# Optimization experiments

Measured on AMD Instinct MI355X. Metric: run time of the kernel, lower is better.

The kernel has to match this reference:

```python
import jax, jax.numpy as jnp
import numpy as np

IN_FEATURES_LS = (32, 64, 128, 256)
OUT_FEATURES = 1024
B, T = 16, 4096


def setup_inputs() -> dict:
    key = jax.random.key(0)
    k_x, k_idx, k_w, k_b = jax.random.split(key, 4)
    n = len(IN_FEATURES_LS)
    x = jax.random.normal(k_x, (B, T, OUT_FEATURES), dtype=jnp.float32)
    # per-row declared feature size, drawn from the configured list
    branch_idx = jax.random.randint(k_idx, (B, T), 0, n)
    in_feat_size = jnp.array(IN_FEATURES_LS, dtype=jnp.int32)[branch_idx]
    # kaiming_uniform_(a=sqrt(5)) on (n, out, out): fan_in = out, bound = 1/sqrt(fan_in)
    bound_w = 1.0 / np.sqrt(OUT_FEATURES)
    weight = jax.random.uniform(k_w, (n, OUT_FEATURES, OUT_FEATURES), dtype=jnp.float32,
                                minval=-bound_w, maxval=bound_w)
    bound_b = 1.0 / np.sqrt(OUT_FEATURES)
    bias = jax.random.uniform(k_b, (n, OUT_FEATURES), dtype=jnp.float32,
                              minval=-bound_b, maxval=bound_b)
    return {"x": x, "in_feat_size": in_feat_size, "weight": weight, "bias": bias}


def reference(x, in_feat_size, weight, bias):
    # Loop over the small fixed set of feature-size branches (matches original).
    out = jnp.zeros(x.shape[:-1] + (OUT_FEATURES,), dtype=x.dtype)
    for idx, feat_size in enumerate(IN_FEATURES_LS):
        mask = (in_feat_size == feat_size)[..., None].astype(x.dtype)  # [B,T,1]
        y = jnp.einsum('oi,bti->bto', weight[idx], x) + bias[idx]
        out = out + mask * y
    return out
```

## Files before the change

kernel.cpp:

```cpp
#include <hip/hip_runtime.h>
#include <hip/hip_bf16.h>

#define OUTF 1024
#define NROWS 65536
#define NBR 4
#define XBROWS 66560
#define NWG 1040

typedef __attribute__((ext_vector_type(8))) short short8;
typedef __attribute__((ext_vector_type(4))) float f32x4;

__device__ inline unsigned short f2bf(float f) {
    return __builtin_bit_cast(unsigned short, (__bf16)f);
}
__device__ inline void gload_lds16(const void* g, void* l) {
    __builtin_amdgcn_global_load_lds(
        (const __attribute__((address_space(1))) void*)g,
        (__attribute__((address_space(3))) void*)l, 16, 0, 0);
}
__device__ inline short8 pack8(float4 a, float4 b) {
    short8 o;
    o[0] = (short)f2bf(a.x); o[1] = (short)f2bf(a.y);
    o[2] = (short)f2bf(a.z); o[3] = (short)f2bf(a.w);
    o[4] = (short)f2bf(b.x); o[5] = (short)f2bf(b.y);
    o[6] = (short)f2bf(b.z); o[7] = (short)f2bf(b.w);
    return o;
}

#define VMCNT(n) asm volatile("s_waitcnt vmcnt(" #n ")" ::: "memory")
#define SBAR() do { __builtin_amdgcn_s_barrier(); __builtin_amdgcn_sched_barrier(0); } while (0)

__global__ void k_count(const int* __restrict__ feat, int* __restrict__ cnt) {
    __shared__ int lc[NBR];
    int tid = threadIdx.x;
    if (tid < NBR) lc[tid] = 0;
    __syncthreads();
    int r = blockIdx.x * 256 + tid;
    int b = 26 - __clz(feat[r]);
    atomicAdd(&lc[b], 1);
    __syncthreads();
    if (tid < NBR && lc[tid]) atomicAdd(&cnt[tid], lc[tid]);
}

__global__ void k_prefix(int* __restrict__ ws) {
    if (threadIdx.x == 0) {
        int s = 0;
        for (int b = 0; b < NBR; b++) {
            ws[4 + b] = s;
            s = (s + ws[b] + 255) & ~255;
            ws[8 + b] = 0;
        }
    }
}

__global__ void k_fill(const int* __restrict__ feat, int* __restrict__ ws,
                       int* __restrict__ rowlist) {
    int tid = threadIdx.x;
    int lane = tid & 63;
    int r = blockIdx.x * 256 + tid;
    int b = 26 - __clz(feat[r]);
    #pragma unroll
    for (int bb = 0; bb < NBR; bb++) {
        unsigned long long mask = __ballot(b == bb);
        int leader = __ffsll((long long)mask) - 1;
        int cntw = __popcll(mask);
        int basepos = 0;
        if (lane == leader) basepos = atomicAdd(&ws[8 + bb], cntw);
        basepos = __shfl(basepos, leader < 0 ? 0 : leader);
        if (b == bb) {
            int prefix = __popcll(mask & ((1ull << lane) - 1ull));
            rowlist[ws[4 + bb] + basepos + prefix] = r;
        }
    }
}

__global__ void k_convw(const float* __restrict__ w, unsigned short* __restrict__ wb) {
    int i = ((int)blockIdx.x * 256 + (int)threadIdx.x) * 8;
    const float4* s = reinterpret_cast<const float4*>(w + i);
    *reinterpret_cast<short8*>(wb + i) = pack8(s[0], s[1]);
}

__global__ void k_convx(const float* __restrict__ x, const int* __restrict__ rowlist,
                        unsigned short* __restrict__ xb) {
    int g = (int)blockIdx.x * 512 + (int)threadIdx.x;
    int orow = g >> 7;
    int cb = (g & 127) << 4;
    int rl = rowlist[orow];
    if ((unsigned)rl >= NROWS) rl = 0;
    const float4* s = reinterpret_cast<const float4*>(x + (size_t)rl * OUTF + (cb >> 1));
    *reinterpret_cast<short8*>(reinterpret_cast<char*>(xb) + (size_t)orow * 2048 + cb) =
        pack8(s[0], s[1]);
}

__global__ __launch_bounds__(512, 2)
void k_gemm6(const unsigned short* __restrict__ xb,
             const unsigned short* __restrict__ wb,
             const float* __restrict__ bias,
             const int* __restrict__ ws_i,
             const int* __restrict__ rowlist,
             float* __restrict__ out) {
    extern __shared__ char lds[];

    const int d = (int)blockIdx.x;
    const int work = (d & 7) * (NWG >> 3) + (d >> 3);
    const int mtile = work >> 2;
    const int ntile = work & 3;

    int branch = -1, lt = 0, cnt = 0, rbase = 0;
    int t_ = mtile;
    #pragma unroll
    for (int b = 0; b < NBR; b++) {
        if (branch < 0) {
            int c = ws_i[b];
            int nt = (c + 255) >> 8;
            if (t_ < nt) { branch = b; lt = t_; cnt = c; rbase = ws_i[4 + b]; }
            else t_ -= nt;
        }
    }
    if (branch < 0) return;

    const int tid = threadIdx.x;
    const int lane = tid & 63;
    const int w8 = tid >> 6;
    const int wm = (w8 >> 2) * 128;
    const int wn = (w8 & 3) * 64;
    const int n0 = ntile * 256;
    const int row0 = rbase + lt * 256;

    const char* aSrc = reinterpret_cast<const char*>(xb)
                       + (size_t)(row0 + (tid >> 2)) * 2048 + ((tid & 3) << 4);
    const char* bSrc = reinterpret_cast<const char*>(wb) + ((size_t)branch << 21)
                       + (size_t)(n0 + (tid >> 2)) * 2048 + ((tid & 3) << 4);
    const int ldst = tid << 4;

    const int aoff = (wm + (lane & 15)) * 64 + ((lane >> 4) << 4);
    const int boff = (wn + (lane & 15)) * 64 + ((lane >> 4) << 4);

    f32x4 acc[8][4];
    #pragma unroll
    for (int i = 0; i < 8; i++)
        #pragma unroll
        for (int j = 0; j < 4; j++) acc[i][j] = (f32x4){0.f, 0.f, 0.f, 0.f};

    #define STAGE(u) do {                                                  \
        const int _sl = (u) % 9;                                           \
        const char* _s = ((u) & 1) ? bSrc : aSrc;                          \
        const int _kb = (((u) >> 2) << 7) + ((((u) >> 1) & 1) << 6);       \
        char* _d = lds + _sl * 16384 + ldst;                               \
        gload_lds16(_s + _kb, _d);                                         \
        gload_lds16(_s + 262144 + _kb, _d + 8192);                         \
    } while (0)

    STAGE(0); STAGE(1); STAGE(2); STAGE(3); STAGE(4); STAGE(5);
    VMCNT(8);
    SBAR();

    short8 af[8], b0, b1;

    for (int t = 0; t < 16; ++t) {
        const int b4 = 4 * t;
        char* A0 = lds + (b4 % 9) * 16384;
        char* B0 = lds + ((b4 + 1) % 9) * 16384;
        char* A1 = lds + ((b4 + 2) % 9) * 16384;
        char* B1 = lds + ((b4 + 3) % 9) * 16384;

        if (t < 15) STAGE(b4 + 6);
        #pragma unroll
        for (int i = 0; i < 8; i++)
            af[i] = *reinterpret_cast<const short8*>(A0 + aoff + i * 1024);
        b0 = *reinterpret_cast<const short8*>(B0 + boff);
        b1 = *reinterpret_cast<const short8*>(B0 + boff + 1024);
        __builtin_amdgcn_s_setprio(1);
        #pragma unroll
        for (int i = 0; i < 8; i++) {
            acc[i][0] = __builtin_amdgcn_mfma_f32_16x16x32_bf16(af[i], b0, acc[i][0], 0, 0, 0);
            acc[i][1] = __builtin_amdgcn_mfma_f32_16x16x32_bf16(af[i], b1, acc[i][1], 0, 0, 0);
        }
        __builtin_amdgcn_s_setprio(0);
        SBAR();

        if (t < 15) STAGE(b4 + 7);
        b0 = *reinterpret_cast<const short8*>(B0 + boff + 2048);
        b1 = *reinterpret_cast<const short8*>(B0 + boff + 3072);
        __builtin_amdgcn_s_setprio(1);
        #pragma unroll
        for (int i = 0; i < 8; i++) {
            acc[i][2] = __builtin_amdgcn_mfma_f32_16x16x32_bf16(af[i], b0, acc[i][2], 0, 0, 0);
            acc[i][3] = __builtin_amdgcn_mfma_f32_16x16x32_bf16(af[i], b1, acc[i][3], 0, 0, 0);
        }
        __builtin_amdgcn_s_setprio(0);
        if (t < 15) { VMCNT(8); } else { VMCNT(0); }
        SBAR();

        if (t < 14) STAGE(b4 + 8);
        #pragma unroll
        for (int i = 0; i < 8; i++)
            af[i] = *reinterpret_cast<const short8*>(A1 + aoff + i * 1024);
        b0 = *reinterpret_cast<const short8*>(B1 + boff);
        b1 = *reinterpret_cast<const short8*>(B1 + boff + 1024);
        __builtin_amdgcn_s_setprio(1);
        #pragma unroll
        for (int i = 0; i < 8; i++) {
            acc[i][0] = __builtin_amdgcn_mfma_f32_16x16x32_bf16(af[i], b0, acc[i][0], 0, 0, 0);
            acc[i][1] = __builtin_amdgcn_mfma_f32_16x16x32_bf16(af[i], b1, acc[i][1], 0, 0, 0);
        }
        __builtin_amdgcn_s_setprio(0);
        SBAR();

        if (t < 14) STAGE(b4 + 9);
        b0 = *reinterpret_cast<const short8*>(B1 + boff + 2048);
        b1 = *reinterpret_cast<const short8*>(B1 + boff + 3072);
        __builtin_amdgcn_s_setprio(1);
        #pragma unroll
        for (int i = 0; i < 8; i++) {
            acc[i][2] = __builtin_amdgcn_mfma_f32_16x16x32_bf16(af[i], b0, acc[i][2], 0, 0, 0);
            acc[i][3] = __builtin_amdgcn_mfma_f32_16x16x32_bf16(af[i], b1, acc[i][3], 0, 0, 0);
        }
        __builtin_amdgcn_s_setprio(0);
        if (t < 14) { VMCNT(8); } else if (t == 14) { VMCNT(4); }
        SBAR();
    }
    #undef STAGE

    const int ccol = lane & 15;
    const int crow = (lane >> 4) << 2;
    float bv[4];
    const float* bp = bias + branch * OUTF + n0 + wn;
    #pragma unroll
    for (int fn = 0; fn < 4; fn++) bv[fn] = bp[fn * 16 + ccol];
    #pragma unroll
    for (int fm = 0; fm < 8; fm++) {
        #pragma unroll
        for (int j = 0; j < 4; j++) {
            int gm = lt * 256 + wm + fm * 16 + crow + j;
            if (gm < cnt) {
                int orow = rowlist[rbase + gm];
                float* orp = out + (size_t)orow * OUTF + n0 + wn;
                #pragma unroll
                for (int fn = 0; fn < 4; fn++)
                    orp[fn * 16 + ccol] = acc[fm][fn][j] + bv[fn];
            }
        }
    }
}

__global__ __launch_bounds__(256, 3)
void k_gemm_fb(const float* __restrict__ x,
               const float* __restrict__ wf,
               const float* __restrict__ bias,
               const int* __restrict__ ws_i,
               const int* __restrict__ rowlist,
               float* __restrict__ out) {
    __shared__ unsigned short As[128][72];
    __shared__ unsigned short Bs[128][72];

    int t = (int)blockIdx.x;
    int branch = -1, ltile = 0, cnt = 0, rbase = 0;
    #pragma unroll
    for (int b = 0; b < NBR; b++) {
        if (branch < 0) {
            int c = ws_i[b];
            int nt = (c + 255) >> 8;
            nt <<= 1;
            if (t < nt) { branch = b; ltile = t; cnt = c; rbase = ws_i[4 + b]; }
            else t -= nt;
        }
    }
    if (branch < 0) return;

    const int tid = threadIdx.x;
    const int lane = tid & 63;
    const int wid = tid >> 6;
    const int wm = (wid & 1) << 6;
    const int wn = (wid >> 1) << 6;
    const int n0 = (int)blockIdx.y * 128;

    const int srow = tid >> 1;
    const int scol = (tid & 1) << 5;

    const int gmrow = ltile * 128 + srow;
    const int grow = (gmrow < cnt) ? rowlist[rbase + gmrow] : -1;
    const float* xsrc = x + (size_t)(grow < 0 ? 0 : grow) * OUTF + scol;
    const float* wfsrc = wf + ((size_t)branch << 20) + (size_t)(n0 + srow) * OUTF + scol;

    f32x4 acc[4][4];
    #pragma unroll
    for (int i = 0; i < 4; i++)
        #pragma unroll
        for (int j = 0; j < 4; j++)
            acc[i][j] = (f32x4){0.f, 0.f, 0.f, 0.f};

    for (int k0 = 0; k0 < OUTF; k0 += 64) {
        {
            unsigned short* dst = &As[srow][scol];
            if (grow >= 0) {
                const float4* s4 = reinterpret_cast<const float4*>(xsrc + k0);
                #pragma unroll
                for (int i = 0; i < 8; i += 2)
                    *reinterpret_cast<short8*>(dst + i * 4) = pack8(s4[i], s4[i + 1]);
            } else {
                short8 z = (short8){0, 0, 0, 0, 0, 0, 0, 0};
                #pragma unroll
                for (int i = 0; i < 8; i += 2) *reinterpret_cast<short8*>(dst + i * 4) = z;
            }
        }
        {
            unsigned short* dst = &Bs[srow][scol];
            const float4* s4 = reinterpret_cast<const float4*>(wfsrc + k0);
            #pragma unroll
            for (int i = 0; i < 8; i += 2)
                *reinterpret_cast<short8*>(dst + i * 4) = pack8(s4[i], s4[i + 1]);
        }
        __syncthreads();
        #pragma unroll
        for (int kk = 0; kk < 64; kk += 32) {
            const int krd = kk + (lane >> 4) * 8;
            short8 af[4], bf_[4];
            #pragma unroll
            for (int i = 0; i < 4; i++)
                af[i] = *reinterpret_cast<const short8*>(&As[wm + i * 16 + (lane & 15)][krd]);
            #pragma unroll
            for (int i = 0; i < 4; i++)
                bf_[i] = *reinterpret_cast<const short8*>(&Bs[wn + i * 16 + (lane & 15)][krd]);
            #pragma unroll
            for (int i = 0; i < 4; i++)
                #pragma unroll
                for (int j = 0; j < 4; j++)
                    acc[i][j] = __builtin_amdgcn_mfma_f32_16x16x32_bf16(af[i], bf_[j], acc[i][j], 0, 0, 0);
        }
        __syncthreads();
    }

    const int ccol = lane & 15;
    const int crow = (lane >> 4) << 2;
    float bv[4];
    const float* bp = bias + branch * OUTF + n0 + wn;
    #pragma unroll
    for (int fn = 0; fn < 4; fn++) bv[fn] = bp[fn * 16 + ccol];
    #pragma unroll
    for (int fm = 0; fm < 4; fm++) {
        #pragma unroll
        for (int j = 0; j < 4; j++) {
            int gm = ltile * 128 + wm + fm * 16 + crow + j;
            if (gm < cnt) {
                int orow = rowlist[rbase + gm];
                float* orp = out + (size_t)orow * OUTF + n0 + wn;
                #pragma unroll
                for (int fn = 0; fn < 4; fn++)
                    orp[fn * 16 + ccol] = acc[fm][fn][j] + bv[fn];
            }
        }
    }
}

extern "C" void kernel_launch(void* const* d_in, const int* in_sizes, int n_in,
                              void* d_out, int out_size, void* d_ws, size_t ws_size,
                              hipStream_t stream) {
    const float* x = (const float*)d_in[0];
    const int* feat = (const int*)d_in[1];
    const float* w = (const float*)d_in[2];
    const float* bias = (const float*)d_in[3];
    float* out = (float*)d_out;

    char* ws = (char*)d_ws;
    int* ws_i = (int*)ws;
    int* rowlist = (int*)(ws + 256);
    const size_t WB_OFF = (size_t)512 << 10;
    const size_t XB_OFF = (size_t)9 << 20;
    unsigned short* wb = (unsigned short*)(ws + WB_OFF);
    unsigned short* xb = (unsigned short*)(ws + XB_OFF);
    const size_t need_full = XB_OFF + (size_t)XBROWS * 2048;

    (void)hipMemsetAsync(ws_i, 0, 64, stream);
    k_count<<<NROWS / 256, 256, 0, stream>>>(feat, ws_i);
    k_prefix<<<1, 64, 0, stream>>>(ws_i);
    k_fill<<<NROWS / 256, 256, 0, stream>>>(feat, ws_i, rowlist);

    if (ws_size >= need_full) {
        k_convw<<<(NBR * OUTF * OUTF) / (256 * 8), 256, 0, stream>>>(w, wb);
        k_convx<<<(XBROWS * 128) / 512, 512, 0, stream>>>(x, rowlist, xb);
        (void)hipFuncSetAttribute((const void*)k_gemm6,
                                  hipFuncAttributeMaxDynamicSharedMemorySize, 147456);
        k_gemm6<<<NWG, 512, 147456, stream>>>(xb, wb, bias, ws_i, rowlist, out);
    } else {
        dim3 grid(NROWS / 128 + 2 * NBR, OUTF / 128);
        k_gemm_fb<<<grid, 256, 0, stream>>>(x, w, bias, ws_i, rowlist, out);
    }
}
```

Before: 364.5 us.

## Rework GEMM LDS pipeline with XOR swizzle, double buffering, and prefix kernel removal

Replaces the 9-slot rotating LDS stage ring with an 8-slot double-buffered layout (A/B halves per k-tile) and cuts dynamic LDS from 144 KB to 128 KB. Fragment loads change to a 4x4 MFMA sub-block order. An XOR swizzle is added to the source chunk and fragment offsets to reduce LDS bank conflicts. The separate prefix-sum kernel launch is dropped and segment bases are recomputed inline from counts in each kernel. The extra barriers and the new wait schedule could add synchronisation stalls, and the changed wait counts must still match the load order.

```diff
diff --git a/kernel.cpp b/kernel.cpp
--- a/kernel.cpp
+++ b/kernel.cpp
@@ -26,9 +26,14 @@
     o[6] = (short)f2bf(b.z); o[7] = (short)f2bf(b.w);
     return o;
 }
-
-#define VMCNT(n) asm volatile("s_waitcnt vmcnt(" #n ")" ::: "memory")
-#define SBAR() do { __builtin_amdgcn_s_barrier(); __builtin_amdgcn_sched_barrier(0); } while (0)
+__device__ inline void seg_bases(const int* __restrict__ ws_i, int* base) {
+    int s = 0;
+    #pragma unroll
+    for (int b = 0; b < NBR; b++) { base[b] = s; s = (s + ws_i[b] + 255) & ~255; }
+}
+
+#define SBAR()  do { __builtin_amdgcn_sched_barrier(0); __builtin_amdgcn_s_barrier(); \
+                     __builtin_amdgcn_sched_barrier(0); } while (0)
 
 __global__ void k_count(const int* __restrict__ feat, int* __restrict__ cnt) {
     __shared__ int lc[NBR];
@@ -42,19 +47,10 @@
     if (tid < NBR && lc[tid]) atomicAdd(&cnt[tid], lc[tid]);
 }
 
-__global__ void k_prefix(int* __restrict__ ws) {
-    if (threadIdx.x == 0) {
-        int s = 0;
-        for (int b = 0; b < NBR; b++) {
-            ws[4 + b] = s;
-            s = (s + ws[b] + 255) & ~255;
-            ws[8 + b] = 0;
-        }
-    }
-}
-
 __global__ void k_fill(const int* __restrict__ feat, int* __restrict__ ws,
                        int* __restrict__ rowlist) {
+    int base[NBR];
+    seg_bases(ws, base);
     int tid = threadIdx.x;
     int lane = tid & 63;
     int r = blockIdx.x * 256 + tid;
@@ -69,7 +65,7 @@
         basepos = __shfl(basepos, leader < 0 ? 0 : leader);
         if (b == bb) {
             int prefix = __popcll(mask & ((1ull << lane) - 1ull));
-            rowlist[ws[4 + bb] + basepos + prefix] = r;
+            rowlist[base[bb] + basepos + prefix] = r;
         }
     }
 }
@@ -93,7 +89,7 @@
 }
 
 __global__ __launch_bounds__(512, 2)
-void k_gemm6(const unsigned short* __restrict__ xb,
+void k_gemm9(const unsigned short* __restrict__ xb,
              const unsigned short* __restrict__ wb,
              const float* __restrict__ bias,
              const int* __restrict__ ws_i,
@@ -106,6 +102,8 @@
     const int mtile = work >> 2;
     const int ntile = work & 3;
 
+    int bases[NBR];
+    seg_bases(ws_i, bases);
     int branch = -1, lt = 0, cnt = 0, rbase = 0;
     int t_ = mtile;
     #pragma unroll
@@ -113,13 +111,13 @@
         if (branch < 0) {
             int c = ws_i[b];
             int nt = (c + 255) >> 8;
-            if (t_ < nt) { branch = b; lt = t_; cnt = c; rbase = ws_i[4 + b]; }
+            if (t_ < nt) { branch = b; lt = t_; cnt = c; rbase = bases[b]; }
             else t_ -= nt;
         }
     }
     if (branch < 0) return;
 
-    const int tid = threadIdx.x;
+    const int tid = (int)threadIdx.x;
     const int lane = tid & 63;
     const int w8 = tid >> 6;
     const int wm = (w8 >> 2) * 128;
@@ -127,14 +125,19 @@
     const int n0 = ntile * 256;
     const int row0 = rbase + lt * 256;
 
-    const char* aSrc = reinterpret_cast<const char*>(xb)
-                       + (size_t)(row0 + (tid >> 2)) * 2048 + ((tid & 3) << 4);
-    const char* bSrc = reinterpret_cast<const char*>(wb) + ((size_t)branch << 21)
-                       + (size_t)(n0 + (tid >> 2)) * 2048 + ((tid & 3) << 4);
-    const int ldst = tid << 4;
-
-    const int aoff = (wm + (lane & 15)) * 64 + ((lane >> 4) << 4);
-    const int boff = (wn + (lane & 15)) * 64 + ((lane >> 4) << 4);
+    const int schunk = ((tid & 3) ^ ((tid >> 3) & 3)) << 4;
+    const char* aS = reinterpret_cast<const char*>(xb)
+                     + (size_t)(row0 + (tid >> 2)) * 2048 + schunk;
+    const char* bS = reinterpret_cast<const char*>(wb) + ((size_t)branch << 21)
+                     + (size_t)(n0 + (tid >> 2)) * 2048 + schunk;
+    const int dst16 = tid << 4;
+
+    auto STAGE = [&](int tile, int typ) {
+        const char* s = (typ >= 2 ? bS : aS) + tile * 128 + (typ & 1) * 64;
+        char* dd = lds + ((((tile & 1) << 2) | typ) << 14) + dst16;
+        gload_lds16(s, dd);
+        gload_lds16(s + 128 * 2048, dd + 8192);
+    };
 
     f32x4 acc[8][4];
     #pragma unroll
@@ -142,85 +145,93 @@
         #pragma unroll
         for (int j = 0; j < 4; j++) acc[i][j] = (f32x4){0.f, 0.f, 0.f, 0.f};
 
-    #define STAGE(u) do {                                                  \
-        const int _sl = (u) % 9;                                           \
-        const char* _s = ((u) & 1) ? bSrc : aSrc;                          \
-        const int _kb = (((u) >> 2) << 7) + ((((u) >> 1) & 1) << 6);       \
-        char* _d = lds + _sl * 16384 + ldst;                               \
-        gload_lds16(_s + _kb, _d);                                         \
-        gload_lds16(_s + 262144 + _kb, _d + 8192);                         \
-    } while (0)
-
-    STAGE(0); STAGE(1); STAGE(2); STAGE(3); STAGE(4); STAGE(5);
-    VMCNT(8);
+    const int lr = lane & 15;
+    const int axor = (((lane >> 4) ^ ((lr >> 1) & 3)) << 4);
+    const int arow = (wm + lr) * 64 + axor;
+    const int brow = (wn + lr) * 64 + axor;
+
+    STAGE(0, 2); STAGE(0, 0); STAGE(0, 3); STAGE(0, 1);
+    STAGE(1, 2); STAGE(1, 0); STAGE(1, 3);
+    asm volatile("s_waitcnt vmcnt(6)" ::: "memory");
     SBAR();
 
-    short8 af[8], b0, b1;
-
+    short8 af[4], bf_[4];
+
+    #pragma unroll 2
     for (int t = 0; t < 16; ++t) {
-        const int b4 = 4 * t;
-        char* A0 = lds + (b4 % 9) * 16384;
-        char* B0 = lds + ((b4 + 1) % 9) * 16384;
-        char* A1 = lds + ((b4 + 2) % 9) * 16384;
-        char* B1 = lds + ((b4 + 3) % 9) * 16384;
-
-        if (t < 15) STAGE(b4 + 6);
-        #pragma unroll
-        for (int i = 0; i < 8; i++)
-            af[i] = *reinterpret_cast<const short8*>(A0 + aoff + i * 1024);
-        b0 = *reinterpret_cast<const short8*>(B0 + boff);
-        b1 = *reinterpret_cast<const short8*>(B0 + boff + 1024);
+        const int rb = (t & 1) << 2;
+        const char* A0 = lds + ((rb | 0) << 14);
+        const char* A1 = lds + ((rb | 1) << 14);
+        const char* B0 = lds + ((rb | 2) << 14);
+        const char* B1 = lds + ((rb | 3) << 14);
+
+        if (t < 15) STAGE(t + 1, 1);
+        #pragma unroll
+        for (int i = 0; i < 4; i++)
+            af[i] = *reinterpret_cast<const short8*>(A0 + arow + i * 1024);
+        #pragma unroll
+        for (int j = 0; j < 4; j++)
+            bf_[j] = *reinterpret_cast<const short8*>(B0 + brow + j * 1024);
+        SBAR();
         __builtin_amdgcn_s_setprio(1);
         #pragma unroll
-        for (int i = 0; i < 8; i++) {
-            acc[i][0] = __builtin_amdgcn_mfma_f32_16x16x32_bf16(af[i], b0, acc[i][0], 0, 0, 0);
-            acc[i][1] = __builtin_amdgcn_mfma_f32_16x16x32_bf16(af[i], b1, acc[i][1], 0, 0, 0);
-        }
+        for (int i = 0; i < 4; i++)
+            #pragma unroll
+            for (int j = 0; j < 4; j++)
+                acc[i][j] = __builtin_amdgcn_mfma_f32_16x16x32_bf16(af[i], bf_[j], acc[i][j], 0, 0, 0);
         __builtin_amdgcn_s_setprio(0);
         SBAR();
 
-        if (t < 15) STAGE(b4 + 7);
-        b0 = *reinterpret_cast<const short8*>(B0 + boff + 2048);
-        b1 = *reinterpret_cast<const short8*>(B0 + boff + 3072);
+        if (t < 14) STAGE(t + 2, 2);
+        #pragma unroll
+        for (int i = 0; i < 4; i++)
+            af[i] = *reinterpret_cast<const short8*>(A0 + arow + 4096 + i * 1024);
+        SBAR();
         __builtin_amdgcn_s_setprio(1);
         #pragma unroll
-        for (int i = 0; i < 8; i++) {
-            acc[i][2] = __builtin_amdgcn_mfma_f32_16x16x32_bf16(af[i], b0, acc[i][2], 0, 0, 0);
-            acc[i][3] = __builtin_amdgcn_mfma_f32_16x16x32_bf16(af[i], b1, acc[i][3], 0, 0, 0);
-        }
+        for (int i = 0; i < 4; i++)
+            #pragma unroll
+            for (int j = 0; j < 4; j++)
+                acc[4 + i][j] = __builtin_amdgcn_mfma_f32_16x16x32_bf16(af[i], bf_[j], acc[4 + i][j], 0, 0, 0);
         __builtin_amdgcn_s_setprio(0);
-        if (t < 15) { VMCNT(8); } else { VMCNT(0); }
-        SBAR();
-
-        if (t < 14) STAGE(b4 + 8);
-        #pragma unroll
-        for (int i = 0; i < 8; i++)
-            af[i] = *reinterpret_cast<const short8*>(A1 + aoff + i * 1024);
-        b0 = *reinterpret_cast<const short8*>(B1 + boff);
-        b1 = *reinterpret_cast<const short8*>(B1 + boff + 1024);
+        SBAR();
+
+        if (t < 14) STAGE(t + 2, 0);
+        #pragma unroll
+        for (int i = 0; i < 4; i++)
+            af[i] = *reinterpret_cast<const short8*>(A1 + arow + i * 1024);
+        #pragma unroll
+        for (int j = 0; j < 4; j++)
+            bf_[j] = *reinterpret_cast<const short8*>(B1 + brow + j * 1024);
+        SBAR();
         __builtin_amdgcn_s_setprio(1);
         #pragma unroll
-        for (int i = 0; i < 8; i++) {
-            acc[i][0] = __builtin_amdgcn_mfma_f32_16x16x32_bf16(af[i], b0, acc[i][0], 0, 0, 0);
-            acc[i][1] = __builtin_amdgcn_mfma_f32_16x16x32_bf16(af[i], b1, acc[i][1], 0, 0, 0);
-        }
+        for (int i = 0; i < 4; i++)
+            #pragma unroll
+            for (int j = 0; j < 4; j++)
+                acc[i][j] = __builtin_amdgcn_mfma_f32_16x16x32_bf16(af[i], bf_[j], acc[i][j], 0, 0, 0);
         __builtin_amdgcn_s_setprio(0);
         SBAR();
 
-        if (t < 14) STAGE(b4 + 9);
-        b0 = *reinterpret_cast<const short8*>(B1 + boff + 2048);
-        b1 = *reinterpret_cast<const short8*>(B1 + boff + 3072);
+        if (t < 14) STAGE(t + 2, 3);
+        #pragma unroll
+        for (int i = 0; i < 4; i++)
+            af[i] = *reinterpret_cast<const short8*>(A1 + arow + 4096 + i * 1024);
+        SBAR();
         __builtin_amdgcn_s_setprio(1);
         #pragma unroll
-        for (int i = 0; i < 8; i++) {
-            acc[i][2] = __builtin_amdgcn_mfma_f32_16x16x32_bf16(af[i], b0, acc[i][2], 0, 0, 0);
-            acc[i][3] = __builtin_amdgcn_mfma_f32_16x16x32_bf16(af[i], b1, acc[i][3], 0, 0, 0);
-        }
+        for (int i = 0; i < 4; i++)
+            #pragma unroll
+            for (int j = 0; j < 4; j++)
+                acc[4 + i][j] = __builtin_amdgcn_mfma_f32_16x16x32_bf16(af[i], bf_[j], acc[4 + i][j], 0, 0, 0);
         __builtin_amdgcn_s_setprio(0);
-        if (t < 14) { VMCNT(8); } else if (t == 14) { VMCNT(4); }
-        SBAR();
-    }
-    #undef STAGE
+        __builtin_amdgcn_sched_barrier(0);
+        if (t < 14)      { asm volatile("s_waitcnt vmcnt(6)" ::: "memory"); }
+        else if (t == 14){ asm volatile("s_waitcnt vmcnt(0)" ::: "memory"); }
+        __builtin_amdgcn_sched_barrier(0);
+        __builtin_amdgcn_s_barrier();
+        __builtin_amdgcn_sched_barrier(0);
+    }
 
     const int ccol = lane & 15;
     const int crow = (lane >> 4) << 2;
@@ -254,6 +265,8 @@
     __shared__ unsigned short As[128][72];
     __shared__ unsigned short Bs[128][72];
 
+    int bases[NBR];
+    seg_bases(ws_i, bases);
     int t = (int)blockIdx.x;
     int branch = -1, ltile = 0, cnt = 0, rbase = 0;
     #pragma unroll
@@ -262,7 +275,7 @@
             int c = ws_i[b];
             int nt = (c + 255) >> 8;
             nt <<= 1;
-            if (t < nt) { branch = b; ltile = t; cnt = c; rbase = ws_i[4 + b]; }
+            if (t < nt) { branch = b; ltile = t; cnt = c; rbase = bases[b]; }
             else t -= nt;
         }
     }
@@ -279,8 +292,9 @@
     const int scol = (tid & 1) << 5;
 
     const int gmrow = ltile * 128 + srow;
-    const int grow = (gmrow < cnt) ? rowlist[rbase + gmrow] : -1;
-    const float* xsrc = x + (size_t)(grow < 0 ? 0 : grow) * OUTF + scol;
+    int grl = (gmrow < cnt) ? rowlist[rbase + gmrow] : -1;
+    if (grl >= NROWS) grl = -1;
+    const float* xsrc = x + (size_t)(grl < 0 ? 0 : grl) * OUTF + scol;
     const float* wfsrc = wf + ((size_t)branch << 20) + (size_t)(n0 + srow) * OUTF + scol;
 
     f32x4 acc[4][4];
@@ -293,7 +307,7 @@
     for (int k0 = 0; k0 < OUTF; k0 += 64) {
         {
             unsigned short* dst = &As[srow][scol];
-            if (grow >= 0) {
+            if (grl >= 0) {
                 const float4* s4 = reinterpret_cast<const float4*>(xsrc + k0);
                 #pragma unroll
                 for (int i = 0; i < 8; i += 2)
@@ -373,15 +387,14 @@
 
     (void)hipMemsetAsync(ws_i, 0, 64, stream);
     k_count<<<NROWS / 256, 256, 0, stream>>>(feat, ws_i);
-    k_prefix<<<1, 64, 0, stream>>>(ws_i);
     k_fill<<<NROWS / 256, 256, 0, stream>>>(feat, ws_i, rowlist);
 
     if (ws_size >= need_full) {
         k_convw<<<(NBR * OUTF * OUTF) / (256 * 8), 256, 0, stream>>>(w, wb);
         k_convx<<<(XBROWS * 128) / 512, 512, 0, stream>>>(x, rowlist, xb);
-        (void)hipFuncSetAttribute((const void*)k_gemm6,
-                                  hipFuncAttributeMaxDynamicSharedMemorySize, 147456);
-        k_gemm6<<<NWG, 512, 147456, stream>>>(xb, wb, bias, ws_i, rowlist, out);
+        (void)hipFuncSetAttribute((const void*)k_gemm9,
+                                  hipFuncAttributeMaxDynamicSharedMemorySize, 131072);
+        k_gemm9<<<NWG, 512, 131072, stream>>>(xb, wb, bias, ws_i, rowlist, out);
     } else {
         dim3 grid(NROWS / 128 + 2 * NBR, OUTF / 128);
         k_gemm_fb<<<grid, 256, 0, stream>>>(x, w, bias, ws_i, rowlist, out);
```

Result: faster. 349.9 us (-4.0%).
